# Kernel optimization log

Hardware: AMD Instinct MI355X
Metric: run time of the kernel (lower is better)

## Reference

```python
import jax, jax.numpy as jnp
import numpy as np

N_NODES = 100000
N_EDGES = 1600000
D_IN = 64
D_HID = 64
N_CLS = 4


def setup_inputs() -> dict:
    key = jax.random.key(0)
    ks = jax.random.split(key, 8)
    s = lambda d: 1.0 / np.sqrt(d)
    return {
        "node_features": jax.random.normal(ks[0], (N_NODES, D_IN), jnp.float32),
        "edge_src": jax.random.randint(ks[1], (N_EDGES,), 0, N_NODES, jnp.int32),
        "edge_dst": jax.random.randint(ks[2], (N_EDGES,), 0, N_NODES, jnp.int32),
        "W_self1": jax.random.normal(ks[3], (D_IN, D_HID), jnp.float32) * s(D_IN),
        "b_self1": jnp.zeros((D_HID,), jnp.float32),
        "W_neigh1": jax.random.normal(ks[4], (D_IN, D_HID), jnp.float32) * s(D_IN),
        "W_self2": jax.random.normal(ks[5], (D_HID, N_CLS), jnp.float32) * s(D_HID),
        "b_self2": jnp.zeros((N_CLS,), jnp.float32),
        "W_neigh2": jax.random.normal(ks[6], (D_HID, N_CLS), jnp.float32) * s(D_HID),
    }


def _sage_mean(h, edge_src, edge_dst, W_self, b_self, W_neigh, n_nodes):
    # mean aggregation over in-neighbors: gather src feats, segment-sum by dst
    msg_sum = jax.ops.segment_sum(h[edge_src], edge_dst, num_segments=n_nodes)
    deg = jax.ops.segment_sum(
        jnp.ones_like(edge_dst, dtype=h.dtype), edge_dst, num_segments=n_nodes
    )
    h_neigh = msg_sum / jnp.maximum(deg, 1.0)[:, None]
    # DGL SAGEConv: fc_self (with bias) + fc_neigh (no bias)
    return h @ W_self + b_self + h_neigh @ W_neigh


def reference(node_features, edge_src, edge_dst, W_self1, b_self1, W_neigh1,
              W_self2, b_self2, W_neigh2):
    n = node_features.shape[0]
    h1 = jnp.tanh(_sage_mean(node_features, edge_src, edge_dst,
                             W_self1, b_self1, W_neigh1, n))
    logits = _sage_mean(h1, edge_src, edge_dst, W_self2, b_self2, W_neigh2, n)
    return logits
```

## Files before the change

### kernel.cpp

```cpp
#include <hip/hip_runtime.h>
#include <hip/hip_bf16.h>
#include <stdint.h>

typedef unsigned char  u8;
typedef unsigned short u16;
typedef unsigned int   u32;
typedef __attribute__((ext_vector_type(8))) short bf16x8;
typedef __attribute__((ext_vector_type(2))) float f32x2;
typedef __attribute__((ext_vector_type(4))) float f32x4;
typedef __attribute__((ext_vector_type(4))) int   i32x4;
typedef __attribute__((ext_vector_type(2))) u32   u32x2;
typedef __attribute__((ext_vector_type(4))) u32   u32x4;

#define BKT_SHIFT 9
#define BKT_NODES 512
#define CAP 12288
#define BINBLK 512
#define GEMMBLK 512

__device__ __forceinline__ float bf2f(u16 u) { return __uint_as_float(((u32)u) << 16); }
__device__ __forceinline__ u16 f2bf(float f) {
    u32 u = __float_as_uint(f);
    u += 0x7FFFu + ((u >> 16) & 1u);
    return (u16)(u >> 16);
}
__device__ __forceinline__ int pkbf(float a, float b) {
    return (int)__builtin_amdgcn_perm(__float_as_uint(b), __float_as_uint(a), 0x07060302u);
}
__device__ __forceinline__ u8 f2fp8(float v) {
    int p = __builtin_amdgcn_cvt_pk_fp8_f32(v, v, 0, false);
    return (u8)(p & 0xff);
}


__global__ __launch_bounds__(256) void k_front(const float* __restrict__ X,
                                               const float* __restrict__ Ws,
                                               const float* __restrict__ b1,
                                               const float* __restrict__ Wn,
                                               u16* __restrict__ Zb,
                                               u8* __restrict__ Y,
                                               int n,
                                               const int* __restrict__ src,
                                               const int* __restrict__ dst,
                                               int* __restrict__ offT,
                                               u32* __restrict__ binned,
                                               int E, int chunk, int nb) {
    __shared__ __align__(16) char sm[31744];
    int t = threadIdx.x;

    if ((int)blockIdx.x < BINBLK) {
        u32* keys = (u32*)sm;
        int* h    = (int*)(sm + 12800);
        int* cur  = (int*)(sm + 13600);
        int* ws4  = (int*)(sm + 14400);
        int blk = blockIdx.x;
        int beg = blk * chunk, end = min(beg + chunk, E), m = max(0, end - beg);

        for (int i = t; i < nb; i += 256) h[i] = 0;
        __syncthreads();
        for (int i = beg + t; i < end; i += 256) atomicAdd(&h[dst[i] >> BKT_SHIFT], 1);
        __syncthreads();
        int v = (t < nb) ? h[t] : 0;
        int lane = t & 63, w = t >> 6;
        int incl = v;
#pragma unroll
        for (int o = 1; o < 64; o <<= 1) {
            int x = __shfl_up(incl, o, 64);
            if (lane >= o) incl += x;
        }
        if (lane == 63) ws4[w] = incl;
        __syncthreads();
        if (t == 0) {
            int run = 0;
#pragma unroll
            for (int i = 0; i < 4; i++) { ws4[4 + i] = run; run += ws4[i]; }
        }
        __syncthreads();
        int excl = incl - v + ws4[4 + w];
        int* orow = offT + (size_t)blk * (nb + 1);
        if (t < nb) { cur[t] = excl; orow[t] = excl; }
        if (t == nb - 1) orow[nb] = excl + v;
        __syncthreads();
        for (int i = beg + t; i < end; i += 256) {
            int d = dst[i], bk = d >> BKT_SHIFT;
            int p = atomicAdd(&cur[bk], 1);
            keys[p] = ((u32)src[i] << BKT_SHIFT) | (u32)(d & (BKT_NODES - 1));
        }
        __syncthreads();
        u32* outp = binned + (size_t)blk * chunk;
        for (int i = t; i < m; i += 256) outp[i] = keys[i];
        return;
    }

    u16* wl = (u16*)sm;
    for (int i = t; i < 8192; i += 256) {
        int k = i >> 7, c = i & 127;
        float wv = (c < 64) ? Ws[k * 64 + c] : Wn[k * 64 + (c - 64)];
        wl[k * 132 + c] = f2bf(wv);
    }
    __syncthreads();

    int wid = t >> 6, lane = t & 63;
    int lrow = lane & 15, lquad = lane >> 4;

    bf16x8 bfrag[8][2];
#pragma unroll
    for (int ct = 0; ct < 8; ct++)
#pragma unroll
        for (int kf = 0; kf < 2; kf++)
#pragma unroll
            for (int j = 0; j < 8; j++)
                bfrag[ct][kf][j] = (short)wl[(kf * 32 + lquad * 8 + j) * 132 + ct * 16 + lrow];

    float bias[4];
#pragma unroll
    for (int ct = 0; ct < 4; ct++) bias[ct] = b1[ct * 16 + lrow];

    u16* Zs = (u16*)(sm + 16896 + wid * 3712);
    u8*  Ys = (u8*)(sm + 16896 + wid * 3712 + 2432);
    int srow = lane >> 2, sseg = lane & 3;

    int tiles = n >> 4;
    int tstride = GEMMBLK * 4;
    for (int tile = (blockIdx.x - BINBLK) * 4 + wid; tile < tiles; tile += tstride) {
        int nb4 = tile << 4;

        const float* xp = X + (size_t)(nb4 + lrow) * 64 + lquad * 8;
        f32x4 x0 = *(const f32x4*)(xp);
        f32x4 x1 = *(const f32x4*)(xp + 4);
        f32x4 x2 = *(const f32x4*)(xp + 32);
        f32x4 x3 = *(const f32x4*)(xp + 36);
        i32x4 p0, p1;
        p0.x = pkbf(x0.x, x0.y); p0.y = pkbf(x0.z, x0.w);
        p0.z = pkbf(x1.x, x1.y); p0.w = pkbf(x1.z, x1.w);
        p1.x = pkbf(x2.x, x2.y); p1.y = pkbf(x2.z, x2.w);
        p1.z = pkbf(x3.x, x3.y); p1.w = pkbf(x3.z, x3.w);
        bf16x8 af0 = __builtin_bit_cast(bf16x8, p0);
        bf16x8 af1 = __builtin_bit_cast(bf16x8, p1);

        f32x4 acc[8];
#pragma unroll
        for (int ct = 0; ct < 8; ct++) {
            f32x4 c = {0.f, 0.f, 0.f, 0.f};
            c = __builtin_amdgcn_mfma_f32_16x16x32_bf16(af0, bfrag[ct][0], c, 0, 0, 0);
            c = __builtin_amdgcn_mfma_f32_16x16x32_bf16(af1, bfrag[ct][1], c, 0, 0, 0);
            acc[ct] = c;
        }

#pragma unroll
        for (int ct = 0; ct < 4; ct++)
#pragma unroll
            for (int r = 0; r < 4; r++)
                Zs[(lquad * 4 + r) * 76 + ct * 16 + lrow] = f2bf(acc[ct][r] + bias[ct]);
#pragma unroll
        for (int ct = 0; ct < 4; ct++)
#pragma unroll
            for (int r = 0; r < 4; r++)
                Ys[(lquad * 4 + r) * 80 + ct * 16 + lrow] = f2fp8(acc[ct + 4][r]);

        u32x4 z0 = *(const u32x4*)&Zs[srow * 76 + sseg * 16];
        u32x4 z1 = *(const u32x4*)&Zs[srow * 76 + sseg * 16 + 8];
        u32x4 yv = *(const u32x4*)&Ys[srow * 80 + sseg * 16];
        *(u32x4*)(Zb + (size_t)(nb4 + srow) * 64 + sseg * 16) = z0;
        *(u32x4*)(Zb + (size_t)(nb4 + srow) * 64 + sseg * 16 + 8) = z1;
        *(u32x4*)(Y + (size_t)(nb4 + srow) * 64 + sseg * 16) = yv;
    }
}


__global__ __launch_bounds__(512) void k_csr(const u32* __restrict__ binned,
                                             const int* __restrict__ offT,
                                             int* __restrict__ rpb,
                                             int* __restrict__ rpe,
                                             int* __restrict__ col,
                                             int chunk, int nb, int n) {
    __shared__ __align__(16) u32 ed[CAP];
    __shared__ u32 srt[CAP];
    __shared__ int gst[BINBLK], gln[BINBLK], soff[BINBLK];
    __shared__ int cnt[BKT_NODES];
    __shared__ int wsum[8], woff[8];
    __shared__ int stot;
    int b = blockIdx.x, t = threadIdx.x;
    int lane = t & 63, w = t >> 6;

    {
        const int* row = offT + (size_t)t * (nb + 1);
        int s = row[b], e = row[b + 1];
        gst[t] = t * chunk + s;
        gln[t] = e - s;
    }
    __syncthreads();
    int v = gln[t];
    int incl = v;
#pragma unroll
    for (int o = 1; o < 64; o <<= 1) {
        int x = __shfl_up(incl, o, 64);
        if (lane >= o) incl += x;
    }
    if (lane == 63) wsum[w] = incl;
    __syncthreads();
    if (t == 0) {
        int run = 0;
#pragma unroll
        for (int i = 0; i < 8; i++) { woff[i] = run; run += wsum[i]; }
        stot = run;
    }
    __syncthreads();
    soff[t] = incl - v + woff[w];
    __syncthreads();
    int total = min(stot, CAP);
    for (int k = w; k < BINBLK; k += 8) {
        int g = gst[k], L = gln[k], o = soff[k];
        for (int i = lane; i < L && o + i < CAP; i += 64) ed[o + i] = binned[g + i];
    }
    cnt[t] = 0;
    __syncthreads();
    for (int i = t; i < total; i += 512)
        atomicAdd(&cnt[ed[i] & (BKT_NODES - 1)], 1);
    __syncthreads();
    int v2 = cnt[t];
    int incl2 = v2;
#pragma unroll
    for (int o = 1; o < 64; o <<= 1) {
        int x = __shfl_up(incl2, o, 64);
        if (lane >= o) incl2 += x;
    }
    if (lane == 63) wsum[w] = incl2;
    __syncthreads();
    if (t == 0) {
        int run = 0;
#pragma unroll
        for (int i = 0; i < 8; i++) { woff[i] = run; run += wsum[i]; }
    }
    __syncthreads();
    int excl2 = incl2 - v2 + woff[w];
    int gnode = b * BKT_NODES + t;
    int cb = b * CAP;
    if (gnode < n) { rpb[gnode] = cb + excl2; rpe[gnode] = cb + excl2 + v2; }
    cnt[t] = excl2;
    __syncthreads();
    for (int i = t; i < total; i += 512) {
        u32 e = ed[i];
        int p = atomicAdd(&cnt[e & (BKT_NODES - 1)], 1);
        srt[p] = e >> BKT_SHIFT;
    }
    __syncthreads();
    for (int i = t; i < total; i += 512) col[cb + i] = (int)srt[i];
}


__global__ __launch_bounds__(256) void k_gather1f(const int* __restrict__ rpb,
                                                  const int* __restrict__ rpe,
                                                  const int* __restrict__ col,
                                                  const u16* __restrict__ Zb,
                                                  const u8* __restrict__ Y,
                                                  const float* __restrict__ Ws2,
                                                  const float* __restrict__ b2,
                                                  const float* __restrict__ Wn2,
                                                  float* __restrict__ P,
                                                  u16* __restrict__ Q, int n) {
    __shared__ float wl[64 * 9];
    int t = threadIdx.x;
    for (int i = t; i < 512; i += 256) {
        int k = i >> 3, c = i & 7;
        float v = (c < 4) ? Ws2[k * 4 + c] : Wn2[k * 4 + (c - 4)];
        wl[((k & 7) * 8 + (k >> 3)) * 9 + c] = v;
    }
    float bb0 = b2[0], bb1 = b2[1], bb2 = b2[2], bb3 = b2[3];
    __syncthreads();

    int w = t >> 6;
    int g = (t >> 3) & 7;
    int l8 = t & 7;
    int node = blockIdx.x * 32 + w * 8 + g;
    if (node >= n) return;

    int beg = rpb[node], end = rpe[node];
    float a[8];
#pragma unroll
    for (int j = 0; j < 8; j++) a[j] = 0.f;

    const u8* yb = Y + (size_t)l8 * 8;
    int e = beg;
    for (; e + 8 <= end; e += 8) {
        i32x4 c0 = *(const i32x4*)(col + e);
        i32x4 c1 = *(const i32x4*)(col + e + 4);
        u32x2 y0 = *(const u32x2*)(yb + (size_t)c0.x * 64);
        u32x2 y1 = *(const u32x2*)(yb + (size_t)c0.y * 64);
        u32x2 y2 = *(const u32x2*)(yb + (size_t)c0.z * 64);
        u32x2 y3 = *(const u32x2*)(yb + (size_t)c0.w * 64);
        u32x2 y4 = *(const u32x2*)(yb + (size_t)c1.x * 64);
        u32x2 y5 = *(const u32x2*)(yb + (size_t)c1.y * 64);
        u32x2 y6 = *(const u32x2*)(yb + (size_t)c1.z * 64);
        u32x2 y7 = *(const u32x2*)(yb + (size_t)c1.w * 64);
#pragma unroll
        for (int j = 0; j < 8; j++) {
            u32x2 yw = (j == 0) ? y0 : (j == 1) ? y1 : (j == 2) ? y2 : (j == 3) ? y3
                     : (j == 4) ? y4 : (j == 5) ? y5 : (j == 6) ? y6 : y7;
            f32x2 lo0 = __builtin_amdgcn_cvt_pk_f32_fp8(yw.x, false);
            f32x2 hi0 = __builtin_amdgcn_cvt_pk_f32_fp8(yw.x, true);
            f32x2 lo1 = __builtin_amdgcn_cvt_pk_f32_fp8(yw.y, false);
            f32x2 hi1 = __builtin_amdgcn_cvt_pk_f32_fp8(yw.y, true);
            a[0] += lo0.x; a[1] += lo0.y; a[2] += hi0.x; a[3] += hi0.y;
            a[4] += lo1.x; a[5] += lo1.y; a[6] += hi1.x; a[7] += hi1.y;
        }
    }
    for (; e + 4 <= end; e += 4) {
        i32x4 cv = *(const i32x4*)(col + e);
        u32x2 y0 = *(const u32x2*)(yb + (size_t)cv.x * 64);
        u32x2 y1 = *(const u32x2*)(yb + (size_t)cv.y * 64);
        u32x2 y2 = *(const u32x2*)(yb + (size_t)cv.z * 64);
        u32x2 y3 = *(const u32x2*)(yb + (size_t)cv.w * 64);
#pragma unroll
        for (int j = 0; j < 4; j++) {
            u32x2 yw = (j == 0) ? y0 : (j == 1) ? y1 : (j == 2) ? y2 : y3;
            f32x2 lo0 = __builtin_amdgcn_cvt_pk_f32_fp8(yw.x, false);
            f32x2 hi0 = __builtin_amdgcn_cvt_pk_f32_fp8(yw.x, true);
            f32x2 lo1 = __builtin_amdgcn_cvt_pk_f32_fp8(yw.y, false);
            f32x2 hi1 = __builtin_amdgcn_cvt_pk_f32_fp8(yw.y, true);
            a[0] += lo0.x; a[1] += lo0.y; a[2] += hi0.x; a[3] += hi0.y;
            a[4] += lo1.x; a[5] += lo1.y; a[6] += hi1.x; a[7] += hi1.y;
        }
    }
    for (; e < end; e++) {
        u32x2 yw = *(const u32x2*)(yb + (size_t)col[e] * 64);
        f32x2 lo0 = __builtin_amdgcn_cvt_pk_f32_fp8(yw.x, false);
        f32x2 hi0 = __builtin_amdgcn_cvt_pk_f32_fp8(yw.x, true);
        f32x2 lo1 = __builtin_amdgcn_cvt_pk_f32_fp8(yw.y, false);
        f32x2 hi1 = __builtin_amdgcn_cvt_pk_f32_fp8(yw.y, true);
        a[0] += lo0.x; a[1] += lo0.y; a[2] += hi0.x; a[3] += hi0.y;
        a[4] += lo1.x; a[5] += lo1.y; a[6] += hi1.x; a[7] += hi1.y;
    }

    float deg = (float)(end - beg);
    float inv = (deg > 0.f) ? 1.f / deg : 0.f;
    u32x4 zr = *(const u32x4*)(Zb + (size_t)node * 64 + l8 * 8);
    float h[8];
#pragma unroll
    for (int j = 0; j < 8; j++) {
        u32 word = (j < 2) ? zr.x : (j < 4) ? zr.y : (j < 6) ? zr.z : zr.w;
        u16 zv = (j & 1) ? (u16)(word >> 16) : (u16)(word & 0xffff);
        h[j] = tanhf(bf2f(zv) + a[j] * inv);
    }

    float r[8];
#pragma unroll
    for (int c = 0; c < 8; c++) r[c] = 0.f;
#pragma unroll
    for (int j = 0; j < 8; j++) {
        float hj = h[j];
        const float* wp = &wl[(j * 8 + l8) * 9];
#pragma unroll
        for (int c = 0; c < 8; c++) r[c] += hj * wp[c];
    }
#pragma unroll
    for (int m = 1; m < 8; m <<= 1)
#pragma unroll
        for (int c = 0; c < 8; c++) r[c] += __shfl_xor(r[c], m, 64);

    if (l8 == 0) {
        *(float4*)(P + (size_t)node * 4) =
            make_float4(r[0] + bb0, r[1] + bb1, r[2] + bb2, r[3] + bb3);
        ushort4 qv;
        qv.x = f2bf(r[4]); qv.y = f2bf(r[5]); qv.z = f2bf(r[6]); qv.w = f2bf(r[7]);
        *(ushort4*)(Q + (size_t)node * 4) = qv;
    }
}


__global__ __launch_bounds__(256) void k_gather2(const int* __restrict__ rpb,
                                                 const int* __restrict__ rpe,
                                                 const int* __restrict__ col,
                                                 const float* __restrict__ P,
                                                 const u16* __restrict__ Q,
                                                 float* __restrict__ out, int n) {
    int t = threadIdx.x;
    int g = t >> 4, l = t & 15;
    int node = blockIdx.x * 16 + g;
    if (node >= n) return;
    int beg = rpb[node], end = rpe[node];
    float a0 = 0.f, a1 = 0.f, a2 = 0.f, a3 = 0.f;
    for (int e = beg + l; e < end; e += 16) {
        ushort4 qv = *(const ushort4*)(Q + (size_t)col[e] * 4);
        a0 += bf2f(qv.x); a1 += bf2f(qv.y); a2 += bf2f(qv.z); a3 += bf2f(qv.w);
    }
#pragma unroll
    for (int m = 1; m < 16; m <<= 1) {
        a0 += __shfl_xor(a0, m, 64);
        a1 += __shfl_xor(a1, m, 64);
        a2 += __shfl_xor(a2, m, 64);
        a3 += __shfl_xor(a3, m, 64);
    }
    if (l == 0) {
        float deg = (float)(end - beg);
        float inv = (deg > 0.f) ? 1.f / deg : 0.f;
        float4 p = *(const float4*)(P + (size_t)node * 4);
        *(float4*)(out + (size_t)node * 4) =
            make_float4(p.x + a0 * inv, p.y + a1 * inv,
                        p.z + a2 * inv, p.w + a3 * inv);
    }
}


extern "C" void kernel_launch(void* const* d_in, const int* in_sizes, int n_in,
                              void* d_out, int out_size, void* d_ws, size_t ws_size,
                              hipStream_t stream) {
    const float* X   = (const float*)d_in[0];
    const int* esrc  = (const int*)d_in[1];
    const int* edst  = (const int*)d_in[2];
    const float* Ws1 = (const float*)d_in[3];
    const float* b1  = (const float*)d_in[4];
    const float* Wn1 = (const float*)d_in[5];
    const float* Ws2 = (const float*)d_in[6];
    const float* b2  = (const float*)d_in[7];
    const float* Wn2 = (const float*)d_in[8];
    float* out = (float*)d_out;

    const int n = in_sizes[0] / 64;
    const int E = in_sizes[1];
    const int nb = (n + BKT_NODES - 1) >> BKT_SHIFT;
    const int chunk = (E + BINBLK - 1) / BINBLK;

    size_t off = 0;
    char* base = (char*)d_ws;
    auto give = [&](size_t bytes) -> char* {
        char* p = base + off;
        off += (bytes + 255) & ~(size_t)255;
        return p;
    };
    int*   offT   = (int*)give((size_t)BINBLK * (nb + 1) * 4);
    int*   rpb    = (int*)give((size_t)n * 4);
    int*   rpe    = (int*)give((size_t)n * 4);
    u32*   binned = (u32*)give((size_t)BINBLK * chunk * 4);
    int*   col    = (int*)give((size_t)nb * CAP * 4);
    u16*   Zb     = (u16*)give((size_t)n * 64 * 2);
    u8*    Y      = (u8*)give((size_t)n * 64);
    float* P      = (float*)give((size_t)n * 4 * 4);
    u16*   Q      = (u16*)give((size_t)n * 4 * 2);

    k_front<<<BINBLK + GEMMBLK, 256, 0, stream>>>(
        X, Ws1, b1, Wn1, Zb, Y, n,
        esrc, edst, offT, binned, E, chunk, nb);

    k_csr<<<nb, 512, 0, stream>>>(binned, offT, rpb, rpe, col, chunk, nb, n);

    k_gather1f<<<(n + 31) / 32, 256, 0, stream>>>(rpb, rpe, col, Zb, Y,
                                                  Ws2, b2, Wn2, P, Q, n);
    k_gather2<<<(n + 15) / 16, 256, 0, stream>>>(rpb, rpe, col, P, Q, out, n);
}
```

Measured before the change: 177.3 us.

## Fuse CSR build with layer-1 gather and halve bucket size

Merges the CSR construction kernel and the first-layer gather/tanh/projection kernel into one, so the sorted source indices are read from LDS instead of being re-read from global memory in a separate launch. Buckets shrink from 512 to 256 nodes (CAP 5120), which doubles the block count and reduces LDS per block, and the binning scan now handles two buckets per thread. The risk is lower occupancy from fusing heavier work into a 512-thread block, and possible overflow if a bucket exceeds the smaller capacity.

```diff
diff --git a/kernel.cpp b/kernel.cpp
--- a/kernel.cpp
+++ b/kernel.cpp
@@ -12,9 +12,9 @@
 typedef __attribute__((ext_vector_type(2))) u32   u32x2;
 typedef __attribute__((ext_vector_type(4))) u32   u32x4;
 
-#define BKT_SHIFT 9
-#define BKT_NODES 512
-#define CAP 12288
+#define BKT_SHIFT 8
+#define BKT_NODES 256
+#define CAP 5120
 #define BINBLK 512
 #define GEMMBLK 512
 
@@ -51,8 +51,8 @@
     if ((int)blockIdx.x < BINBLK) {
         u32* keys = (u32*)sm;
         int* h    = (int*)(sm + 12800);
-        int* cur  = (int*)(sm + 13600);
-        int* ws4  = (int*)(sm + 14400);
+        int* cur  = (int*)(sm + 14400);
+        int* ws4  = (int*)(sm + 16000);
         int blk = blockIdx.x;
         int beg = blk * chunk, end = min(beg + chunk, E), m = max(0, end - beg);
 
@@ -60,9 +60,12 @@
         __syncthreads();
         for (int i = beg + t; i < end; i += 256) atomicAdd(&h[dst[i] >> BKT_SHIFT], 1);
         __syncthreads();
-        int v = (t < nb) ? h[t] : 0;
         int lane = t & 63, w = t >> 6;
-        int incl = v;
+        int e0 = 2 * t, e1 = 2 * t + 1;
+        int h0 = (e0 < nb) ? h[e0] : 0;
+        int h1 = (e1 < nb) ? h[e1] : 0;
+        int s = h0 + h1;
+        int incl = s;
 #pragma unroll
         for (int o = 1; o < 64; o <<= 1) {
             int x = __shfl_up(incl, o, 64);
@@ -76,10 +79,11 @@
             for (int i = 0; i < 4; i++) { ws4[4 + i] = run; run += ws4[i]; }
         }
         __syncthreads();
-        int excl = incl - v + ws4[4 + w];
+        int excl = incl - s + ws4[4 + w];
         int* orow = offT + (size_t)blk * (nb + 1);
-        if (t < nb) { cur[t] = excl; orow[t] = excl; }
-        if (t == nb - 1) orow[nb] = excl + v;
+        if (e0 < nb) { cur[e0] = excl;      orow[e0] = excl; }
+        if (e1 < nb) { cur[e1] = excl + h0; orow[e1] = excl + h0; }
+        if (t == 255) orow[nb] = excl + s;
         __syncthreads();
         for (int i = beg + t; i < end; i += 256) {
             int d = dst[i], bk = d >> BKT_SHIFT;
@@ -168,28 +172,43 @@
 }
 
 
-__global__ __launch_bounds__(512) void k_csr(const u32* __restrict__ binned,
-                                             const int* __restrict__ offT,
-                                             int* __restrict__ rpb,
-                                             int* __restrict__ rpe,
-                                             int* __restrict__ col,
-                                             int chunk, int nb, int n) {
+__global__ __launch_bounds__(512) void k_csrg1(const u32* __restrict__ binned,
+                                               const int* __restrict__ offT,
+                                               const u16* __restrict__ Zb,
+                                               const u8* __restrict__ Y,
+                                               const float* __restrict__ Ws2,
+                                               const float* __restrict__ b2,
+                                               const float* __restrict__ Wn2,
+                                               int* __restrict__ rpb,
+                                               int* __restrict__ rpe,
+                                               int* __restrict__ col,
+                                               float* __restrict__ P,
+                                               u16* __restrict__ Q,
+                                               int chunk, int nb, int n) {
     __shared__ __align__(16) u32 ed[CAP];
-    __shared__ u32 srt[CAP];
+    __shared__ __align__(16) u32 srt[CAP];
     __shared__ int gst[BINBLK], gln[BINBLK], soff[BINBLK];
     __shared__ int cnt[BKT_NODES];
+    __shared__ float wl[64 * 9];
     __shared__ int wsum[8], woff[8];
     __shared__ int stot;
     int b = blockIdx.x, t = threadIdx.x;
     int lane = t & 63, w = t >> 6;
 
+    {
+        int k = t >> 3, c = t & 7;
+        float v = (c < 4) ? Ws2[k * 4 + c] : Wn2[k * 4 + (c - 4)];
+        wl[((k & 7) * 8 + (k >> 3)) * 9 + c] = v;
+    }
     {
         const int* row = offT + (size_t)t * (nb + 1);
         int s = row[b], e = row[b + 1];
         gst[t] = t * chunk + s;
         gln[t] = e - s;
     }
-    __syncthreads();
+    float bb0 = b2[0], bb1 = b2[1], bb2 = b2[2], bb3 = b2[3];
+    __syncthreads();
+
     int v = gln[t];
     int incl = v;
 #pragma unroll
@@ -209,16 +228,23 @@
     soff[t] = incl - v + woff[w];
     __syncthreads();
     int total = min(stot, CAP);
-    for (int k = w; k < BINBLK; k += 8) {
-        int g = gst[k], L = gln[k], o = soff[k];
-        for (int i = lane; i < L && o + i < CAP; i += 64) ed[o + i] = binned[g + i];
-    }
-    cnt[t] = 0;
-    __syncthreads();
+
+    {
+        int sg = lane >> 3, sl = lane & 7;
+        for (int k0 = w * 8 + sg; k0 < BINBLK; k0 += 64) {
+            int g = gst[k0], L = gln[k0], o = soff[k0];
+            for (int i = sl; i < L; i += 8)
+                if (o + i < CAP) ed[o + i] = binned[g + i];
+        }
+    }
+    if (t < BKT_NODES) cnt[t] = 0;
+    __syncthreads();
+
     for (int i = t; i < total; i += 512)
         atomicAdd(&cnt[ed[i] & (BKT_NODES - 1)], 1);
     __syncthreads();
-    int v2 = cnt[t];
+
+    int v2 = (t < BKT_NODES) ? cnt[t] : 0;
     int incl2 = v2;
 #pragma unroll
     for (int o = 1; o < 64; o <<= 1) {
@@ -234,69 +260,57 @@
     }
     __syncthreads();
     int excl2 = incl2 - v2 + woff[w];
-    int gnode = b * BKT_NODES + t;
     int cb = b * CAP;
-    if (gnode < n) { rpb[gnode] = cb + excl2; rpe[gnode] = cb + excl2 + v2; }
-    cnt[t] = excl2;
-    __syncthreads();
+    if (t < BKT_NODES) {
+        int gnode = b * BKT_NODES + t;
+        if (gnode < n) { rpb[gnode] = cb + excl2; rpe[gnode] = cb + excl2 + v2; }
+        gst[t] = excl2;
+        gln[t] = v2;
+        cnt[t] = excl2;
+    }
+    __syncthreads();
+
     for (int i = t; i < total; i += 512) {
         u32 e = ed[i];
         int p = atomicAdd(&cnt[e & (BKT_NODES - 1)], 1);
         srt[p] = e >> BKT_SHIFT;
     }
     __syncthreads();
+
     for (int i = t; i < total; i += 512) col[cb + i] = (int)srt[i];
-}
-
-
-__global__ __launch_bounds__(256) void k_gather1f(const int* __restrict__ rpb,
-                                                  const int* __restrict__ rpe,
-                                                  const int* __restrict__ col,
-                                                  const u16* __restrict__ Zb,
-                                                  const u8* __restrict__ Y,
-                                                  const float* __restrict__ Ws2,
-                                                  const float* __restrict__ b2,
-                                                  const float* __restrict__ Wn2,
-                                                  float* __restrict__ P,
-                                                  u16* __restrict__ Q, int n) {
-    __shared__ float wl[64 * 9];
-    int t = threadIdx.x;
-    for (int i = t; i < 512; i += 256) {
-        int k = i >> 3, c = i & 7;
-        float v = (c < 4) ? Ws2[k * 4 + c] : Wn2[k * 4 + (c - 4)];
-        wl[((k & 7) * 8 + (k >> 3)) * 9 + c] = v;
-    }
-    float bb0 = b2[0], bb1 = b2[1], bb2 = b2[2], bb3 = b2[3];
-    __syncthreads();
-
-    int w = t >> 6;
-    int g = (t >> 3) & 7;
-    int l8 = t & 7;
-    int node = blockIdx.x * 32 + w * 8 + g;
-    if (node >= n) return;
-
-    int beg = rpb[node], end = rpe[node];
-    float a[8];
-#pragma unroll
-    for (int j = 0; j < 8; j++) a[j] = 0.f;
-
+
+    int gid = t >> 3, l8 = t & 7;
     const u8* yb = Y + (size_t)l8 * 8;
-    int e = beg;
-    for (; e + 8 <= end; e += 8) {
-        i32x4 c0 = *(const i32x4*)(col + e);
-        i32x4 c1 = *(const i32x4*)(col + e + 4);
-        u32x2 y0 = *(const u32x2*)(yb + (size_t)c0.x * 64);
-        u32x2 y1 = *(const u32x2*)(yb + (size_t)c0.y * 64);
-        u32x2 y2 = *(const u32x2*)(yb + (size_t)c0.z * 64);
-        u32x2 y3 = *(const u32x2*)(yb + (size_t)c0.w * 64);
-        u32x2 y4 = *(const u32x2*)(yb + (size_t)c1.x * 64);
-        u32x2 y5 = *(const u32x2*)(yb + (size_t)c1.y * 64);
-        u32x2 y6 = *(const u32x2*)(yb + (size_t)c1.z * 64);
-        u32x2 y7 = *(const u32x2*)(yb + (size_t)c1.w * 64);
-#pragma unroll
-        for (int j = 0; j < 8; j++) {
-            u32x2 yw = (j == 0) ? y0 : (j == 1) ? y1 : (j == 2) ? y2 : (j == 3) ? y3
-                     : (j == 4) ? y4 : (j == 5) ? y5 : (j == 6) ? y6 : y7;
+#pragma unroll 1
+    for (int r = 0; r < 4; r++) {
+        int ln_ = gid + r * 64;
+        int node = b * BKT_NODES + ln_;
+        if (node >= n) continue;
+        int s0 = gst[ln_], L = gln[ln_];
+        float a[8];
+#pragma unroll
+        for (int j = 0; j < 8; j++) a[j] = 0.f;
+        int e = 0;
+        for (; e + 8 <= L; e += 8) {
+            int s_[8];
+#pragma unroll
+            for (int j = 0; j < 8; j++) s_[j] = (int)srt[s0 + e + j];
+            u32x2 y_[8];
+#pragma unroll
+            for (int j = 0; j < 8; j++) y_[j] = *(const u32x2*)(yb + (size_t)s_[j] * 64);
+#pragma unroll
+            for (int j = 0; j < 8; j++) {
+                f32x2 lo0 = __builtin_amdgcn_cvt_pk_f32_fp8(y_[j].x, false);
+                f32x2 hi0 = __builtin_amdgcn_cvt_pk_f32_fp8(y_[j].x, true);
+                f32x2 lo1 = __builtin_amdgcn_cvt_pk_f32_fp8(y_[j].y, false);
+                f32x2 hi1 = __builtin_amdgcn_cvt_pk_f32_fp8(y_[j].y, true);
+                a[0] += lo0.x; a[1] += lo0.y; a[2] += hi0.x; a[3] += hi0.y;
+                a[4] += lo1.x; a[5] += lo1.y; a[6] += hi1.x; a[7] += hi1.y;
+            }
+        }
+        for (; e < L; e++) {
+            int sj = (int)srt[s0 + e];
+            u32x2 yw = *(const u32x2*)(yb + (size_t)sj * 64);
             f32x2 lo0 = __builtin_amdgcn_cvt_pk_f32_fp8(yw.x, false);
             f32x2 hi0 = __builtin_amdgcn_cvt_pk_f32_fp8(yw.x, true);
             f32x2 lo1 = __builtin_amdgcn_cvt_pk_f32_fp8(yw.y, false);
@@ -304,66 +318,40 @@
             a[0] += lo0.x; a[1] += lo0.y; a[2] += hi0.x; a[3] += hi0.y;
             a[4] += lo1.x; a[5] += lo1.y; a[6] += hi1.x; a[7] += hi1.y;
         }
-    }
-    for (; e + 4 <= end; e += 4) {
-        i32x4 cv = *(const i32x4*)(col + e);
-        u32x2 y0 = *(const u32x2*)(yb + (size_t)cv.x * 64);
-        u32x2 y1 = *(const u32x2*)(yb + (size_t)cv.y * 64);
-        u32x2 y2 = *(const u32x2*)(yb + (size_t)cv.z * 64);
-        u32x2 y3 = *(const u32x2*)(yb + (size_t)cv.w * 64);
-#pragma unroll
-        for (int j = 0; j < 4; j++) {
-            u32x2 yw = (j == 0) ? y0 : (j == 1) ? y1 : (j == 2) ? y2 : y3;
-            f32x2 lo0 = __builtin_amdgcn_cvt_pk_f32_fp8(yw.x, false);
-            f32x2 hi0 = __builtin_amdgcn_cvt_pk_f32_fp8(yw.x, true);
-            f32x2 lo1 = __builtin_amdgcn_cvt_pk_f32_fp8(yw.y, false);
-            f32x2 hi1 = __builtin_amdgcn_cvt_pk_f32_fp8(yw.y, true);
-            a[0] += lo0.x; a[1] += lo0.y; a[2] += hi0.x; a[3] += hi0.y;
-            a[4] += lo1.x; a[5] += lo1.y; a[6] += hi1.x; a[7] += hi1.y;
-        }
-    }
-    for (; e < end; e++) {
-        u32x2 yw = *(const u32x2*)(yb + (size_t)col[e] * 64);
-        f32x2 lo0 = __builtin_amdgcn_cvt_pk_f32_fp8(yw.x, false);
-        f32x2 hi0 = __builtin_amdgcn_cvt_pk_f32_fp8(yw.x, true);
-        f32x2 lo1 = __builtin_amdgcn_cvt_pk_f32_fp8(yw.y, false);
-        f32x2 hi1 = __builtin_amdgcn_cvt_pk_f32_fp8(yw.y, true);
-        a[0] += lo0.x; a[1] += lo0.y; a[2] += hi0.x; a[3] += hi0.y;
-        a[4] += lo1.x; a[5] += lo1.y; a[6] += hi1.x; a[7] += hi1.y;
-    }
-
-    float deg = (float)(end - beg);
-    float inv = (deg > 0.f) ? 1.f / deg : 0.f;
-    u32x4 zr = *(const u32x4*)(Zb + (size_t)node * 64 + l8 * 8);
-    float h[8];
-#pragma unroll
-    for (int j = 0; j < 8; j++) {
-        u32 word = (j < 2) ? zr.x : (j < 4) ? zr.y : (j < 6) ? zr.z : zr.w;
-        u16 zv = (j & 1) ? (u16)(word >> 16) : (u16)(word & 0xffff);
-        h[j] = tanhf(bf2f(zv) + a[j] * inv);
-    }
-
-    float r[8];
-#pragma unroll
-    for (int c = 0; c < 8; c++) r[c] = 0.f;
-#pragma unroll
-    for (int j = 0; j < 8; j++) {
-        float hj = h[j];
-        const float* wp = &wl[(j * 8 + l8) * 9];
-#pragma unroll
-        for (int c = 0; c < 8; c++) r[c] += hj * wp[c];
-    }
-#pragma unroll
-    for (int m = 1; m < 8; m <<= 1)
-#pragma unroll
-        for (int c = 0; c < 8; c++) r[c] += __shfl_xor(r[c], m, 64);
-
-    if (l8 == 0) {
-        *(float4*)(P + (size_t)node * 4) =
-            make_float4(r[0] + bb0, r[1] + bb1, r[2] + bb2, r[3] + bb3);
-        ushort4 qv;
-        qv.x = f2bf(r[4]); qv.y = f2bf(r[5]); qv.z = f2bf(r[6]); qv.w = f2bf(r[7]);
-        *(ushort4*)(Q + (size_t)node * 4) = qv;
+
+        float deg = (float)L;
+        float inv = (deg > 0.f) ? 1.f / deg : 0.f;
+        u32x4 zr = *(const u32x4*)(Zb + (size_t)node * 64 + l8 * 8);
+        float h[8];
+#pragma unroll
+        for (int j = 0; j < 8; j++) {
+            u32 word = (j < 2) ? zr.x : (j < 4) ? zr.y : (j < 6) ? zr.z : zr.w;
+            u16 zv = (j & 1) ? (u16)(word >> 16) : (u16)(word & 0xffff);
+            h[j] = tanhf(bf2f(zv) + a[j] * inv);
+        }
+
+        float rr[8];
+#pragma unroll
+        for (int c = 0; c < 8; c++) rr[c] = 0.f;
+#pragma unroll
+        for (int j = 0; j < 8; j++) {
+            float hj = h[j];
+            const float* wp = &wl[(j * 8 + l8) * 9];
+#pragma unroll
+            for (int c = 0; c < 8; c++) rr[c] += hj * wp[c];
+        }
+#pragma unroll
+        for (int m = 1; m < 8; m <<= 1)
+#pragma unroll
+            for (int c = 0; c < 8; c++) rr[c] += __shfl_xor(rr[c], m, 64);
+
+        if (l8 == 0) {
+            *(float4*)(P + (size_t)node * 4) =
+                make_float4(rr[0] + bb0, rr[1] + bb1, rr[2] + bb2, rr[3] + bb3);
+            ushort4 qv;
+            qv.x = f2bf(rr[4]); qv.y = f2bf(rr[5]); qv.z = f2bf(rr[6]); qv.w = f2bf(rr[7]);
+            *(ushort4*)(Q + (size_t)node * 4) = qv;
+        }
     }
 }
 
@@ -442,9 +430,8 @@
         X, Ws1, b1, Wn1, Zb, Y, n,
         esrc, edst, offT, binned, E, chunk, nb);
 
-    k_csr<<<nb, 512, 0, stream>>>(binned, offT, rpb, rpe, col, chunk, nb, n);
-
-    k_gather1f<<<(n + 31) / 32, 256, 0, stream>>>(rpb, rpe, col, Zb, Y,
-                                                  Ws2, b2, Wn2, P, Q, n);
+    k_csrg1<<<nb, 512, 0, stream>>>(binned, offT, Zb, Y, Ws2, b2, Wn2,
+                                    rpb, rpe, col, P, Q, chunk, nb, n);
+
     k_gather2<<<(n + 15) / 16, 256, 0, stream>>>(rpb, rpe, col, P, Q, out, n);
 }
```

Result: faster. 157.3 us (median of 2 runs) (-11.3%).
